# Kernel tuning notes

Hardware: AMD Instinct MI355X
Metric: run time of the kernel (lower is better)

Reference implementation:

```python
import jax, jax.numpy as jnp
import numpy as np

NPOINT, RADIUS, NSAMPLE = 512, 0.2, 32
BN_EPS = 1e-5


def square_distance(src, dst):
    # src: (B,N,3), dst: (B,M,3) -> (B,M,N)
    d = -2.0 * jnp.einsum('bmc,bnc->bmn', dst, src)
    d = d + jnp.sum(dst ** 2, -1)[:, :, None]
    d = d + jnp.sum(src ** 2, -1)[:, None, :]
    return d


def farthest_point_sample(xyz, npoint):
    B, N, _ = xyz.shape
    def step(carry, _):
        distance, farthest = carry
        centroid = jnp.take_along_axis(xyz, farthest[:, None, None], axis=1)  # (B,1,3)
        dist = jnp.sum((xyz - centroid) ** 2, -1)  # (B,N)
        distance = jnp.minimum(distance, dist)
        return (distance, jnp.argmax(distance, -1)), farthest
    init = (jnp.full((B, N), 1e10, dtype=xyz.dtype), jnp.zeros((B,), dtype=jnp.int32))
    _, idx = jax.lax.scan(step, init, None, length=npoint)
    return idx.T  # (B, npoint)


def ball_query(radius, nsample, xyz, new_xyz):
    sqr = square_distance(xyz, new_xyz)  # (B,S,N)
    mask = sqr > radius ** 2
    d = jnp.where(mask, 1e10, sqr)
    group_idx = jnp.argsort(d, axis=-1)[:, :, :nsample]  # (B,S,K)
    group_first = jnp.broadcast_to(group_idx[:, :, :1], group_idx.shape)
    cond = (jnp.sum(mask, -1) < nsample)[:, :, None]
    return jnp.where(cond, group_first, group_idx)


def index_points(points, idx):
    # points: (B,N,C), idx: (B,...) -> (B,...,C)
    return jax.vmap(lambda p, i: p[i])(points, idx)


def setup_inputs() -> dict:
    key = jax.random.key(0)
    ks = jax.random.split(key, 20)
    B, N, C = 16, 4096, 64
    xyz = jax.random.normal(ks[0], (B, N, 3), dtype=jnp.float32)
    points = jax.random.normal(ks[1], (B, N, C), dtype=jnp.float32)
    chans = [C + 3, 64, 64, 128]
    inp = {'xyz': xyz, 'points': points}
    for i in range(3):
        cin, cout = chans[i], chans[i + 1]
        inp[f'w{i}'] = jax.random.normal(ks[2 + 4 * i], (cout, cin), dtype=jnp.float32) * (1.0 / np.sqrt(cin))
        inp[f'b{i}'] = jax.random.normal(ks[3 + 4 * i], (cout,), dtype=jnp.float32) * 0.01
        inp[f'gamma{i}'] = jnp.ones((cout,), dtype=jnp.float32)
        inp[f'beta{i}'] = jnp.zeros((cout,), dtype=jnp.float32)
        inp[f'rmean{i}'] = jax.random.normal(ks[4 + 4 * i], (cout,), dtype=jnp.float32) * 0.01
        inp[f'rvar{i}'] = jnp.ones((cout,), dtype=jnp.float32)
    return inp


def reference(xyz, points,
              w0, b0, gamma0, beta0, rmean0, rvar0,
              w1, b1, gamma1, beta1, rmean1, rvar1,
              w2, b2, gamma2, beta2, rmean2, rvar2):
    fps_idx = farthest_point_sample(xyz, NPOINT)            # (B,S)
    new_xyz = index_points(xyz, fps_idx)                    # (B,S,3)
    group_idx = ball_query(RADIUS, NSAMPLE, xyz, new_xyz)   # (B,S,K)
    grouped_xyz = index_points(xyz, group_idx)              # (B,S,K,3)
    grouped_xyz_norm = grouped_xyz - new_xyz[:, :, None, :]
    grouped_points = index_points(points, group_idx)        # (B,S,K,C)
    new_points = jnp.concatenate([grouped_xyz_norm, grouped_points], axis=-1)
    x = jnp.transpose(new_points, (0, 3, 1, 2))             # (B,C+3,S,K)
    for w, b, g, be, rm, rv in ((w0, b0, gamma0, beta0, rmean0, rvar0),
                                (w1, b1, gamma1, beta1, rmean1, rvar1),
                                (w2, b2, gamma2, beta2, rmean2, rvar2)):
        x = jnp.einsum('bcsk,oc->bosk', x, w) + b[None, :, None, None]
        x = (x - rm[None, :, None, None]) * jax.lax.rsqrt(rv + BN_EPS)[None, :, None, None]
        x = x * g[None, :, None, None] + be[None, :, None, None]
        x = jax.nn.relu(x)
    new_points_out = jnp.max(x, axis=3)                     # (B,Cout,S)
    new_points_out = jnp.transpose(new_points_out, (0, 2, 1))
    return new_xyz, new_points_out
```

## Files before the change

kernel.cpp:

```cpp
#include <hip/hip_runtime.h>
#include <hip/hip_bf16.h>
#include <math.h>

#define BB 16
#define NN 4096
#define SS 512
#define KK 32
#define CC 64
#define KCAP 2048

typedef _Float16 f16x8 __attribute__((ext_vector_type(8)));
typedef float f32x4 __attribute__((ext_vector_type(4)));

template <int CTRL>
__device__ __forceinline__ unsigned long long dpp_umax64(unsigned long long k) {
  int lo = (int)(unsigned)(k & 0xFFFFFFFFull);
  int hi = (int)(unsigned)(k >> 32);
  int tlo = __builtin_amdgcn_update_dpp(lo, lo, CTRL, 0xF, 0xF, false);
  int thi = __builtin_amdgcn_update_dpp(hi, hi, CTRL, 0xF, 0xF, false);
  unsigned long long t = ((unsigned long long)(unsigned)thi << 32) | (unsigned)tlo;
  return t > k ? t : k;
}

__global__ __launch_bounds__(512) void fps_kernel(const float* __restrict__ xyz,
                                                  float* __restrict__ newxyz) {
#pragma clang fp contract(off)
  const int b = blockIdx.x, tid = threadIdx.x;
  const int wid = tid >> 6, lane = tid & 63;
  __shared__ float sx[NN], sy[NN], sz[NN];
  __shared__ unsigned long long cand[2][8];
  __shared__ int sel[SS];
  const float* base = xyz + (size_t)b * NN * 3;
  for (int p = tid; p < NN; p += 512) {
    sx[p] = base[3 * p + 0];
    sy[p] = base[3 * p + 1];
    sz[p] = base[3 * p + 2];
  }
  if (tid == 0) sel[0] = 0;
  __syncthreads();
  float px[8], py[8], pz[8], d[8];
#pragma unroll
  for (int j = 0; j < 8; j++) {
    int p = tid * 8 + j;
    px[j] = sx[p]; py[j] = sy[p]; pz[j] = sz[p];
    d[j] = 1e10f;
  }
  float cx = sx[0], cy = sy[0], cz = sz[0];
  for (int it = 0; it < SS - 1; it++) {
    float bv = -1.0f;
    int bj = 0;
#pragma unroll
    for (int j = 0; j < 8; j++) {
      float dx = px[j] - cx, dy = py[j] - cy, dz = pz[j] - cz;
      float t0 = dx * dx, t1 = dy * dy, t2 = dz * dz;
      float dd = (t0 + t1) + t2;
      float nd = fminf(d[j], dd);
      d[j] = nd;
      if (nd > bv) { bv = nd; bj = j; }
    }
    const int bp = tid * 8 + bj;
    unsigned long long key =
        ((unsigned long long)__float_as_uint(bv) << 32) | (unsigned)(NN - 1 - bp);
    key = dpp_umax64<0x111>(key);
    key = dpp_umax64<0x112>(key);
    key = dpp_umax64<0x114>(key);
    key = dpp_umax64<0x118>(key);
    key = dpp_umax64<0x142>(key);
    key = dpp_umax64<0x143>(key);
    const int par = it & 1;
    if (lane == 63) cand[par][wid] = key;
    __syncthreads();
    unsigned long long k = cand[par][lane & 7];
    k = dpp_umax64<0x111>(k);
    k = dpp_umax64<0x112>(k);
    k = dpp_umax64<0x114>(k);
    const int lo = __builtin_amdgcn_readlane((int)(unsigned)(k & 0xFFFFFFFFull), 7);
    const int cur = NN - 1 - lo;
    cx = sx[cur]; cy = sy[cur]; cz = sz[cur];
    if (tid == 0) sel[it + 1] = cur;
  }
  __syncthreads();
  for (int i = tid; i < SS * 3; i += 512) {
    int s = i / 3, c = i - s * 3;
    int g = sel[s];
    float v = (c == 0) ? sx[g] : (c == 1) ? sy[g] : sz[g];
    newxyz[((size_t)b * SS + s) * 3 + c] = v;
  }
}

__global__ __launch_bounds__(256) void ballq_kernel(const float* __restrict__ xyz,
                                                    const float* __restrict__ newxyz,
                                                    int* __restrict__ gidx) {
#pragma clang fp contract(off)
  const int bs = blockIdx.x;
  const int b = bs >> 9;
  const int tid = threadIdx.x;
  __shared__ unsigned long long keys[KCAP];
  __shared__ int s_cnt;
  __shared__ unsigned char inflag[64];
  __shared__ int outg[KK];
  __shared__ unsigned long long rk[4];
  __shared__ int rp[4];
  if (tid == 0) s_cnt = 0;
  __syncthreads();
  const float cx = newxyz[bs * 3 + 0];
  const float cy = newxyz[bs * 3 + 1];
  const float cz = newxyz[bs * 3 + 2];
  const float csq = (cx * cx + cy * cy) + cz * cz;
  const float* base = xyz + (size_t)b * NN * 3;
  const float R2 = 0.04f;
  float4 f[12];
  {
    const float4* b4 = reinterpret_cast<const float4*>(base) + tid * 12;
#pragma unroll
    for (int s = 0; s < 12; s++) f[s] = b4[s];
  }
#define BQ_ELEM(e) ((e & 3) == 0 ? f[(e) >> 2].x : (e & 3) == 1 ? f[(e) >> 2].y \
                  : (e & 3) == 2 ? f[(e) >> 2].z : f[(e) >> 2].w)
#pragma unroll
  for (int mIdx = 0; mIdx < 16; mIdx++) {
    const int p = tid * 16 + mIdx;
    float x = BQ_ELEM(3 * mIdx + 0);
    float y = BQ_ELEM(3 * mIdx + 1);
    float z = BQ_ELEM(3 * mIdx + 2);
    float dot = (cx * x + cy * y) + cz * z;
    float ssq = (x * x + y * y) + z * z;
    float dsq = ((-2.0f * dot) + csq) + ssq;
    bool in = !(dsq > R2);
    if (p < 64) inflag[p] = in ? (unsigned char)1 : (unsigned char)0;
    if (in) {
      int pos = atomicAdd(&s_cnt, 1);
      unsigned u = __float_as_uint(dsq);
      u ^= (u >> 31) ? 0xFFFFFFFFu : 0x80000000u;
      if (pos < KCAP)
        keys[pos] = ((unsigned long long)u << 32) | (unsigned)p;
    }
  }
#undef BQ_ELEM
  __syncthreads();
  const int cnt = s_cnt;

  if (cnt > KCAP) {
    if (tid == 0) {
      unsigned long long best[KK];
      for (int i = 0; i < KK; i++) best[i] = ~0ull;
      for (int p = 0; p < NN; p++) {
        float x = base[3 * p + 0], y = base[3 * p + 1], z = base[3 * p + 2];
        float dot = (cx * x + cy * y) + cz * z;
        float ssq = (x * x + y * y) + z * z;
        float dsq = ((-2.0f * dot) + csq) + ssq;
        if (!(dsq > R2)) {
          unsigned u = __float_as_uint(dsq);
          u ^= (u >> 31) ? 0xFFFFFFFFu : 0x80000000u;
          unsigned long long key = ((unsigned long long)u << 32) | (unsigned)p;
          if (key < best[KK - 1]) {
            int ins = KK - 1;
            while (ins > 0 && best[ins - 1] > key) { best[ins] = best[ins - 1]; ins--; }
            best[ins] = key;
          }
        }
      }
      if (NN - cnt < KK) {
        for (int i = 0; i < KK; i++) outg[i] = (int)(best[0] & 0xFFFFFFFFull);
      } else {
        for (int i = 0; i < KK; i++) outg[i] = (int)(best[i] & 0xFFFFFFFFull);
      }
    }
  } else if (cnt <= KK) {
    if (tid < cnt && tid < KK) outg[tid] = (int)(keys[tid] & 0xFFFFFFFFull);
    if (tid == 0) {
      int pos = cnt;
      for (int i = 0; i < 64 && pos < KK; i++)
        if (!inflag[i]) outg[pos++] = i;
    }
  } else {
    for (int r = 0; r < KK; r++) {
      unsigned long long mk = ~0ull; int mp = -1;
      for (int i = tid; i < cnt; i += 256)
        if (keys[i] < mk) { mk = keys[i]; mp = i; }
      for (int off = 1; off < 64; off <<= 1) {
        unsigned long long ok = __shfl_xor(mk, off);
        int op = __shfl_xor(mp, off);
        if (ok < mk) { mk = ok; mp = op; }
      }
      if ((tid & 63) == 0) { rk[tid >> 6] = mk; rp[tid >> 6] = mp; }
      __syncthreads();
      if (tid == 0) {
        unsigned long long fm = rk[0]; int fp = rp[0];
        for (int i = 1; i < 4; i++) if (rk[i] < fm) { fm = rk[i]; fp = rp[i]; }
        outg[r] = (int)(fm & 0xFFFFFFFFull);
        keys[fp] = ~0ull;
      }
      __syncthreads();
    }
  }
  __syncthreads();
  if (tid < KK) gidx[(size_t)bs * KK + tid] = outg[tid];
}

__device__ __forceinline__ f32x4 mfma16(f16x8 a, f16x8 b, f32x4 c) {
  return __builtin_amdgcn_mfma_f32_16x16x32_f16(a, b, c, 0, 0, 0);
}

template <int KS, int NT, bool LAST>
__device__ __forceinline__ void mfma_layer(
    const int tid, _Float16 (*Xh)[104], _Float16 (*Wh)[104],
    float* sa, float* sbv, float (*mmp)[4],
    const float* __restrict__ w, const float* __restrict__ bb,
    const float* __restrict__ gg, const float* __restrict__ be,
    const float* __restrict__ rm, const float* __restrict__ rv,
    const int CIN, const bool permute_l0,
    float* __restrict__ out2, const int bs0) {
  constexpr int COUT = NT * 16;
  const int wid = tid >> 6, lane = tid & 63;
  const int w32 = wid * 32;
  if (tid < COUT) {
    float a = gg[tid] / sqrtf(rv[tid] + 1e-5f);
    sa[tid] = a;
    sbv[tid] = (bb[tid] - rm[tid]) * a + be[tid];
  }
  __syncthreads();
  for (int i = tid; i < COUT * CIN; i += 256) {
    int oc = i / CIN;
    int c = i - oc * CIN;
    int col = permute_l0 ? ((c < 3) ? 64 + c : c - 3) : c;
    Wh[oc][col] = (_Float16)(w[i] * sa[oc]);
  }
  __syncthreads();
  f32x4 acc[2][NT];
#pragma unroll
  for (int mt = 0; mt < 2; mt++)
#pragma unroll
    for (int nt = 0; nt < NT; nt++) acc[mt][nt] = (f32x4){0.f, 0.f, 0.f, 0.f};
  const int r15 = lane & 15, kg = (lane >> 4) * 8;
#pragma unroll
  for (int ks = 0; ks < KS; ks++) {
    const int kk = ks * 32 + kg;
    f16x8 a0 = *(const f16x8*)&Xh[w32 + r15][kk];
    f16x8 a1 = *(const f16x8*)&Xh[w32 + 16 + r15][kk];
#pragma unroll
    for (int nt = 0; nt < NT; nt++) {
      f16x8 bf = *(const f16x8*)&Wh[nt * 16 + r15][kk];
      acc[0][nt] = mfma16(a0, bf, acc[0][nt]);
      acc[1][nt] = mfma16(a1, bf, acc[1][nt]);
    }
  }
  __syncthreads();
  if constexpr (!LAST) {
#pragma unroll
    for (int nt = 0; nt < NT; nt++) {
      const int col = nt * 16 + r15;
      const float bias = sbv[col];
#pragma unroll
      for (int mt = 0; mt < 2; mt++)
#pragma unroll
        for (int r = 0; r < 4; r++) {
          const int row = w32 + mt * 16 + (lane >> 4) * 4 + r;
          Xh[row][col] = (_Float16)fmaxf(acc[mt][nt][r] + bias, 0.0f);
        }
    }
  } else {
#pragma unroll
    for (int nt = 0; nt < NT; nt++) {
      const int col = nt * 16 + r15;
      const float bias = sbv[col];
      float mx = 0.0f;
#pragma unroll
      for (int mt = 0; mt < 2; mt++)
#pragma unroll
        for (int r = 0; r < 4; r++)
          mx = fmaxf(mx, fmaxf(acc[mt][nt][r] + bias, 0.0f));
      mmp[wid * 128 + col][lane >> 4] = mx;
    }
    __syncthreads();
    for (int e = tid; e < 4 * 128; e += 256) {
      float m = fmaxf(fmaxf(mmp[e][0], mmp[e][1]), fmaxf(mmp[e][2], mmp[e][3]));
      out2[((size_t)(bs0 + (e >> 7))) * 128 + (e & 127)] = m;
    }
  }
}

__global__ __launch_bounds__(256, 2) void mlp_kernel(
    const float* __restrict__ xyz, const float* __restrict__ points,
    const float* __restrict__ newxyz, const int* __restrict__ gidx,
    const float* __restrict__ w0, const float* __restrict__ b0,
    const float* __restrict__ g0, const float* __restrict__ be0,
    const float* __restrict__ rm0, const float* __restrict__ rv0,
    const float* __restrict__ w1, const float* __restrict__ b1,
    const float* __restrict__ g1, const float* __restrict__ be1,
    const float* __restrict__ rm1, const float* __restrict__ rv1,
    const float* __restrict__ w2, const float* __restrict__ b2,
    const float* __restrict__ g2, const float* __restrict__ be2,
    const float* __restrict__ rm2, const float* __restrict__ rv2,
    float* __restrict__ out2) {
  const int tid = threadIdx.x;
  const int bs0 = blockIdx.x * 4;
  const int b = bs0 >> 9;
  __shared__ _Float16 Xh[128][104];
  __shared__ _Float16 Wh[128][104];
  __shared__ float sa[128], sbv[128];
  __shared__ float mmp[512][4];
  __shared__ int sg[128];
  if (tid < 128) sg[tid] = gidx[(size_t)bs0 * KK + tid];
  __syncthreads();
  for (int i = tid; i < 128 * 16; i += 256) {
    int r = i >> 4, c4 = i & 15;
    float4 v = *reinterpret_cast<const float4*>(
        &points[((size_t)b * NN + sg[r]) * CC + c4 * 4]);
    _Float16* dst = &Xh[r][c4 * 4];
    dst[0] = (_Float16)v.x; dst[1] = (_Float16)v.y;
    dst[2] = (_Float16)v.z; dst[3] = (_Float16)v.w;
  }
  if (tid < 128) {
    int ci = tid >> 5;
    int g = sg[tid];
    const float* cp = newxyz + ((size_t)bs0 + ci) * 3;
    const float* pp = xyz + ((size_t)b * NN + g) * 3;
    Xh[tid][64] = (_Float16)(pp[0] - cp[0]);
    Xh[tid][65] = (_Float16)(pp[1] - cp[1]);
    Xh[tid][66] = (_Float16)(pp[2] - cp[2]);
  }
  for (int i = tid; i < 128 * 29; i += 256) {
    int r = i / 29, c = 67 + i % 29;
    Xh[r][c] = (_Float16)0.0f;
    if (r < 64) Wh[r][c] = (_Float16)0.0f;
  }
  mfma_layer<3, 4, false>(tid, Xh, Wh, sa, sbv, mmp, w0, b0, g0, be0, rm0, rv0,
                          67, true, nullptr, bs0);
  mfma_layer<2, 4, false>(tid, Xh, Wh, sa, sbv, mmp, w1, b1, g1, be1, rm1, rv1,
                          64, false, nullptr, bs0);
  mfma_layer<2, 8, true>(tid, Xh, Wh, sa, sbv, mmp, w2, b2, g2, be2, rm2, rv2,
                         64, false, out2, bs0);
}

extern "C" void kernel_launch(void* const* d_in, const int* in_sizes, int n_in,
                              void* d_out, int out_size, void* d_ws, size_t ws_size,
                              hipStream_t stream) {
  const float* xyz = (const float*)d_in[0];
  const float* points = (const float*)d_in[1];
  const float* w0 = (const float*)d_in[2];
  const float* b0 = (const float*)d_in[3];
  const float* g0 = (const float*)d_in[4];
  const float* be0 = (const float*)d_in[5];
  const float* rm0 = (const float*)d_in[6];
  const float* rv0 = (const float*)d_in[7];
  const float* w1 = (const float*)d_in[8];
  const float* b1 = (const float*)d_in[9];
  const float* g1 = (const float*)d_in[10];
  const float* be1 = (const float*)d_in[11];
  const float* rm1 = (const float*)d_in[12];
  const float* rv1 = (const float*)d_in[13];
  const float* w2 = (const float*)d_in[14];
  const float* b2 = (const float*)d_in[15];
  const float* g2 = (const float*)d_in[16];
  const float* be2 = (const float*)d_in[17];
  const float* rm2 = (const float*)d_in[18];
  const float* rv2 = (const float*)d_in[19];

  float* newxyz = (float*)d_out;
  float* out2 = (float*)d_out + (size_t)BB * SS * 3;
  int* gidx = (int*)d_ws;

  fps_kernel<<<BB, 512, 0, stream>>>(xyz, newxyz);
  ballq_kernel<<<BB * SS, 256, 0, stream>>>(xyz, newxyz, gidx);
  mlp_kernel<<<(BB * SS) / 4, 256, 0, stream>>>(
      xyz, points, newxyz, gidx,
      w0, b0, g0, be0, rm0, rv0,
      w1, b1, g1, be1, rm1, rv1,
      w2, b2, g2, be2, rm2, rv2,
      out2);
}
```

Measured before the change: 437.1 us.

## Process two batches per FPS block to interleave independent reduction chains

```diff
diff --git a/kernel.cpp b/kernel.cpp
--- a/kernel.cpp
+++ b/kernel.cpp
@@ -25,66 +25,92 @@
 __global__ __launch_bounds__(512) void fps_kernel(const float* __restrict__ xyz,
                                                   float* __restrict__ newxyz) {
 #pragma clang fp contract(off)
-  const int b = blockIdx.x, tid = threadIdx.x;
+  const int b0 = blockIdx.x * 2, tid = threadIdx.x;
   const int wid = tid >> 6, lane = tid & 63;
-  __shared__ float sx[NN], sy[NN], sz[NN];
-  __shared__ unsigned long long cand[2][8];
-  __shared__ int sel[SS];
-  const float* base = xyz + (size_t)b * NN * 3;
+  __shared__ float sxA[NN], syA[NN], szA[NN];
+  __shared__ float sxB[NN], syB[NN], szB[NN];
+  __shared__ unsigned long long candA[2][8], candB[2][8];
+  __shared__ int selA[SS], selB[SS];
+  const float* baseA = xyz + (size_t)b0 * NN * 3;
+  const float* baseB = xyz + (size_t)(b0 + 1) * NN * 3;
   for (int p = tid; p < NN; p += 512) {
-    sx[p] = base[3 * p + 0];
-    sy[p] = base[3 * p + 1];
-    sz[p] = base[3 * p + 2];
-  }
-  if (tid == 0) sel[0] = 0;
-  __syncthreads();
-  float px[8], py[8], pz[8], d[8];
+    sxA[p] = baseA[3 * p + 0];
+    syA[p] = baseA[3 * p + 1];
+    szA[p] = baseA[3 * p + 2];
+    sxB[p] = baseB[3 * p + 0];
+    syB[p] = baseB[3 * p + 1];
+    szB[p] = baseB[3 * p + 2];
+  }
+  if (tid == 0) { selA[0] = 0; selB[0] = 0; }
+  __syncthreads();
+  float pxA[8], pyA[8], pzA[8], dA[8];
+  float pxB[8], pyB[8], pzB[8], dB[8];
 #pragma unroll
   for (int j = 0; j < 8; j++) {
     int p = tid * 8 + j;
-    px[j] = sx[p]; py[j] = sy[p]; pz[j] = sz[p];
-    d[j] = 1e10f;
-  }
-  float cx = sx[0], cy = sy[0], cz = sz[0];
+    pxA[j] = sxA[p]; pyA[j] = syA[p]; pzA[j] = szA[p]; dA[j] = 1e10f;
+    pxB[j] = sxB[p]; pyB[j] = syB[p]; pzB[j] = szB[p]; dB[j] = 1e10f;
+  }
+  float cxA = sxA[0], cyA = syA[0], czA = szA[0];
+  float cxB = sxB[0], cyB = syB[0], czB = szB[0];
   for (int it = 0; it < SS - 1; it++) {
-    float bv = -1.0f;
-    int bj = 0;
+    float bvA = -1.0f; int bjA = 0;
 #pragma unroll
     for (int j = 0; j < 8; j++) {
-      float dx = px[j] - cx, dy = py[j] - cy, dz = pz[j] - cz;
+      float dx = pxA[j] - cxA, dy = pyA[j] - cyA, dz = pzA[j] - czA;
       float t0 = dx * dx, t1 = dy * dy, t2 = dz * dz;
       float dd = (t0 + t1) + t2;
-      float nd = fminf(d[j], dd);
-      d[j] = nd;
-      if (nd > bv) { bv = nd; bj = j; }
-    }
-    const int bp = tid * 8 + bj;
-    unsigned long long key =
-        ((unsigned long long)__float_as_uint(bv) << 32) | (unsigned)(NN - 1 - bp);
-    key = dpp_umax64<0x111>(key);
-    key = dpp_umax64<0x112>(key);
-    key = dpp_umax64<0x114>(key);
-    key = dpp_umax64<0x118>(key);
-    key = dpp_umax64<0x142>(key);
-    key = dpp_umax64<0x143>(key);
+      float nd = fminf(dA[j], dd);
+      dA[j] = nd;
+      if (nd > bvA) { bvA = nd; bjA = j; }
+    }
+    float bvB = -1.0f; int bjB = 0;
+#pragma unroll
+    for (int j = 0; j < 8; j++) {
+      float dx = pxB[j] - cxB, dy = pyB[j] - cyB, dz = pzB[j] - czB;
+      float t0 = dx * dx, t1 = dy * dy, t2 = dz * dz;
+      float dd = (t0 + t1) + t2;
+      float nd = fminf(dB[j], dd);
+      dB[j] = nd;
+      if (nd > bvB) { bvB = nd; bjB = j; }
+    }
+    unsigned long long keyA =
+        ((unsigned long long)__float_as_uint(bvA) << 32) | (unsigned)(NN - 1 - (tid * 8 + bjA));
+    unsigned long long keyB =
+        ((unsigned long long)__float_as_uint(bvB) << 32) | (unsigned)(NN - 1 - (tid * 8 + bjB));
+    keyA = dpp_umax64<0x111>(keyA); keyB = dpp_umax64<0x111>(keyB);
+    keyA = dpp_umax64<0x112>(keyA); keyB = dpp_umax64<0x112>(keyB);
+    keyA = dpp_umax64<0x114>(keyA); keyB = dpp_umax64<0x114>(keyB);
+    keyA = dpp_umax64<0x118>(keyA); keyB = dpp_umax64<0x118>(keyB);
+    keyA = dpp_umax64<0x142>(keyA); keyB = dpp_umax64<0x142>(keyB);
+    keyA = dpp_umax64<0x143>(keyA); keyB = dpp_umax64<0x143>(keyB);
     const int par = it & 1;
-    if (lane == 63) cand[par][wid] = key;
+    if (lane == 63) {
+      candA[par][wid] = keyA;
+      candB[par][wid] = keyB;
+    }
     __syncthreads();
-    unsigned long long k = cand[par][lane & 7];
-    k = dpp_umax64<0x111>(k);
-    k = dpp_umax64<0x112>(k);
-    k = dpp_umax64<0x114>(k);
-    const int lo = __builtin_amdgcn_readlane((int)(unsigned)(k & 0xFFFFFFFFull), 7);
-    const int cur = NN - 1 - lo;
-    cx = sx[cur]; cy = sy[cur]; cz = sz[cur];
-    if (tid == 0) sel[it + 1] = cur;
+    unsigned long long kA = candA[par][lane & 7];
+    unsigned long long kB = candB[par][lane & 7];
+    kA = dpp_umax64<0x111>(kA); kB = dpp_umax64<0x111>(kB);
+    kA = dpp_umax64<0x112>(kA); kB = dpp_umax64<0x112>(kB);
+    kA = dpp_umax64<0x114>(kA); kB = dpp_umax64<0x114>(kB);
+    const int loA = __builtin_amdgcn_readlane((int)(unsigned)(kA & 0xFFFFFFFFull), 7);
+    const int loB = __builtin_amdgcn_readlane((int)(unsigned)(kB & 0xFFFFFFFFull), 7);
+    const int curA = NN - 1 - loA;
+    const int curB = NN - 1 - loB;
+    cxA = sxA[curA]; cyA = syA[curA]; czA = szA[curA];
+    cxB = sxB[curB]; cyB = syB[curB]; czB = szB[curB];
+    if (tid == 0) { selA[it + 1] = curA; selB[it + 1] = curB; }
   }
   __syncthreads();
   for (int i = tid; i < SS * 3; i += 512) {
     int s = i / 3, c = i - s * 3;
-    int g = sel[s];
-    float v = (c == 0) ? sx[g] : (c == 1) ? sy[g] : sz[g];
-    newxyz[((size_t)b * SS + s) * 3 + c] = v;
+    int gA = selA[s], gB = selB[s];
+    float vA = (c == 0) ? sxA[gA] : (c == 1) ? syA[gA] : szA[gA];
+    float vB = (c == 0) ? sxB[gB] : (c == 1) ? syB[gB] : szB[gB];
+    newxyz[((size_t)b0 * SS + s) * 3 + c] = vA;
+    newxyz[((size_t)(b0 + 1) * SS + s) * 3 + c] = vB;
   }
 }
 
@@ -361,7 +387,7 @@
   float* out2 = (float*)d_out + (size_t)BB * SS * 3;
   int* gidx = (int*)d_ws;
 
-  fps_kernel<<<BB, 512, 0, stream>>>(xyz, newxyz);
+  fps_kernel<<<BB / 2, 512, 0, stream>>>(xyz, newxyz);
   ballq_kernel<<<BB * SS, 256, 0, stream>>>(xyz, newxyz, gidx);
   mlp_kernel<<<(BB * SS) / 4, 256, 0, stream>>>(
       xyz, points, newxyz, gidx,
```

After: 680.6 us. +55.7%, slower.
